# Kernel optimization log

Hardware: AMD Instinct MI355X
Metric: run time of the kernel (lower is better)

Reference implementation:

```python
import jax, jax.numpy as jnp
import numpy as np

N_NODES = 50000
N_EDGES = 800000
D = 256


def setup_inputs() -> dict:
    key = jax.random.key(0)
    k_x, k_e, k_w1, k_w2 = jax.random.split(key, 4)
    x = jax.random.normal(k_x, (N_NODES, D), dtype=jnp.float32)
    edge_index = jax.random.randint(k_e, (2, N_EDGES), 0, N_NODES, dtype=jnp.int64)
    # attention MLP params (Linear(d, d//2) -> ReLU -> Linear(d//2, 1) -> Sigmoid)
    W1 = jax.random.normal(k_w1, (D, D // 2), dtype=jnp.float32) * (1.0 / np.sqrt(D))
    b1 = jnp.zeros((D // 2,), dtype=jnp.float32)
    W2 = jax.random.normal(k_w2, (D // 2, 1), dtype=jnp.float32) * (1.0 / np.sqrt(D // 2))
    b2 = jnp.zeros((1,), dtype=jnp.float32)
    return {"x": x, "edge_index": edge_index, "W1": W1, "b1": b1, "W2": W2, "b2": b2}


def reference(x, edge_index, W1, b1, W2, b2):
    # mean aggregation with attention: for each destination node i (row),
    # weighted mean of neighbor (col) features with sigmoid-MLP attention weights.
    row, col = edge_index[0], edge_index[1]
    neigh = x[col]                                   # [E, D] gathered neighbor features
    h = jax.nn.relu(neigh @ W1 + b1)                 # [E, D//2]
    w = jax.nn.sigmoid(h @ W2 + b2)                  # [E, 1] attention weight per edge
    num = jax.ops.segment_sum(neigh * w, row, num_segments=N_NODES)  # [N, D]
    den = jax.ops.segment_sum(w, row, num_segments=N_NODES)          # [N, 1]
    # nodes with no neighbors stay zero (matching the torch loop's skip)
    out = jnp.where(den > 0, num / jnp.maximum(den, 1e-12), 0.0)
    return out
```

## Files before the change

### kernel.cpp

```cpp
#include <hip/hip_runtime.h>
#include <hip/hip_bf16.h>

#define D 256
#define DH 128
#define NB 8

typedef __attribute__((ext_vector_type(8))) short short8;
typedef __attribute__((ext_vector_type(4))) float floatx4;

__device__ __forceinline__ int eload(const void* p, long long i, int is64) {
    if (is64) return (int)((const long long*)p)[i];
    return ((const int*)p)[i];
}

__device__ __forceinline__ unsigned pack_bf16(unsigned a, unsigned b) {
    unsigned ra = (a + 0x7fffu + ((a >> 16) & 1u)) >> 16;
    unsigned rb = (b + 0x7fffu + ((b >> 16) & 1u)) & 0xffff0000u;
    return ra | rb;
}
__device__ __forceinline__ unsigned short bf16_of(float f) {
    unsigned u = __float_as_uint(f);
    return (unsigned short)((u + 0x7fffu + ((u >> 16) & 1u)) >> 16);
}

__global__ __launch_bounds__(256) void prep_kernel(const float* __restrict__ W1,
                                                   uint4* __restrict__ Bp,
                                                   const int* __restrict__ ei,
                                                   int* __restrict__ flag, int E) {
    if (blockIdx.x == 16) {
        int tid = threadIdx.x;
        int limit = min(E, 4096);
        int v = 0;
        for (int i = tid; i < limit; i += 256) v |= ei[2 * i + 1];
#pragma unroll
        for (int off = 32; off > 0; off >>= 1) v |= __shfl_down(v, off, 64);
        if ((tid & 63) == 0) atomicOr(flag, v);
        return;
    }
    int t = blockIdx.x * 256 + threadIdx.x;
    int lane = t & 63;
    int kt = (t >> 6) & 7;
    int nt = t >> 9;
    int col = nt * 16 + (lane & 15);
    int k0 = kt * 32 + (lane >> 4) * 8;
    unsigned v[8];
#pragma unroll
    for (int j = 0; j < 8; ++j) v[j] = __float_as_uint(W1[(k0 + j) * DH + col]);
    uint4 o;
    o.x = pack_bf16(v[0], v[1]);
    o.y = pack_bf16(v[2], v[3]);
    o.z = pack_bf16(v[4], v[5]);
    o.w = pack_bf16(v[6], v[7]);
    Bp[t] = o;
}

__global__ __launch_bounds__(256) void score_scatter_kernel(
        const float* __restrict__ x, const uint4* __restrict__ Bp,
        const float* __restrict__ b1, const float* __restrict__ W2,
        const float* __restrict__ b2, uint2* __restrict__ xb,
        float* __restrict__ s,
        const void* __restrict__ ep, const int* __restrict__ flag,
        int* __restrict__ cursor, unsigned short* __restrict__ cols,
        int cap, int pad, int N, int E, int SB) {
    if ((int)blockIdx.x >= SB) {
        int is64 = (*flag == 0);
        int base = (blockIdx.x - SB) * 1024 + threadIdx.x;
        int r[4], c[4];
        bool vld[4];
#pragma unroll
        for (int j = 0; j < 4; ++j) {
            int e = base + j * 256;
            vld[j] = (e < E);
            if (vld[j]) {
                r[j] = eload(ep, e, is64);
                c[j] = eload(ep, (long long)E + e, is64);
            }
        }
#pragma unroll
        for (int j = 0; j < 4; ++j) {
            if (vld[j]) {
                int p = atomicAdd(&cursor[r[j] * pad], 1);
                if (p < cap) cols[(size_t)r[j] * cap + p] = (unsigned short)c[j];
            }
        }
        return;
    }

    __shared__ __align__(16) uint2 lds[64 * 65];
    int tid = threadIdx.x;
    int blk = blockIdx.x;
    long long n64 = (long long)N * 64;

    long long gbase = (long long)blk * 4096 + tid;
#pragma unroll
    for (int i = 0; i < 16; ++i) {
        long long g = gbase + i * 256;
        int idx = i * 256 + tid;
        if (g < n64) {
            uint4 f = ((const uint4*)x)[g];
            uint2 o;
            o.x = pack_bf16(f.x, f.y);
            o.y = pack_bf16(f.z, f.w);
            xb[g] = o;
            lds[(idx >> 6) * 65 + (idx & 63)] = o;
        }
    }
    __syncthreads();

    int lane = tid & 63;
    int wid = tid >> 6;
    int quad = lane >> 4;
    int rbase = blk * 64 + wid * 16;
    int lrow = wid * 16 + (lane & 15);

    short8 afrag[8];
#pragma unroll
    for (int kt = 0; kt < 8; ++kt)
        afrag[kt] = *(const short8*)&lds[lrow * 65 + kt * 8 + quad * 2];

    float z0 = 0.f, z1 = 0.f, z2 = 0.f, z3 = 0.f;
#pragma unroll
    for (int nt = 0; nt < 8; ++nt) {
        floatx4 acc = {0.f, 0.f, 0.f, 0.f};
#pragma unroll
        for (int kt = 0; kt < 8; ++kt) {
            uint4 braw = Bp[(nt * 8 + kt) * 64 + lane];
            short8 b;
            b.s0 = (short)(braw.x & 0xffff); b.s1 = (short)(braw.x >> 16);
            b.s2 = (short)(braw.y & 0xffff); b.s3 = (short)(braw.y >> 16);
            b.s4 = (short)(braw.z & 0xffff); b.s5 = (short)(braw.z >> 16);
            b.s6 = (short)(braw.w & 0xffff); b.s7 = (short)(braw.w >> 16);
            acc = __builtin_amdgcn_mfma_f32_16x16x32_bf16(afrag[kt], b, acc, 0, 0, 0);
        }
        int col = nt * 16 + (lane & 15);
        float b1c = b1[col], w2c = W2[col];
        z0 += fmaxf(acc[0] + b1c, 0.f) * w2c;
        z1 += fmaxf(acc[1] + b1c, 0.f) * w2c;
        z2 += fmaxf(acc[2] + b1c, 0.f) * w2c;
        z3 += fmaxf(acc[3] + b1c, 0.f) * w2c;
    }

#pragma unroll
    for (int off = 1; off < 16; off <<= 1) {
        z0 += __shfl_xor(z0, off, 64);
        z1 += __shfl_xor(z1, off, 64);
        z2 += __shfl_xor(z2, off, 64);
        z3 += __shfl_xor(z3, off, 64);
    }
    if ((lane & 15) == 0) {
        float b2v = b2[0];
        int r = rbase + quad * 4;
        float zz[4] = {z0, z1, z2, z3};
#pragma unroll
        for (int j = 0; j < 4; ++j)
            if (r + j < N) s[r + j] = 1.f / (1.f + __expf(-(zz[j] + b2v)));
    }
}

__device__ __forceinline__ float4 unpack_bf16x4(uint2 v) {
    float4 r;
    r.x = __uint_as_float(v.x << 16);
    r.y = __uint_as_float(v.x & 0xffff0000u);
    r.z = __uint_as_float(v.y << 16);
    r.w = __uint_as_float(v.y & 0xffff0000u);
    return r;
}

__global__ __launch_bounds__(256) void agg_u16_kernel(const uint2* __restrict__ xb,
                                                      const float* __restrict__ s,
                                                      const int* __restrict__ cursor,
                                                      const unsigned short* __restrict__ cols,
                                                      int cap, int pad,
                                                      float4* __restrict__ out4, int N) {
    int lane = threadIdx.x & 63;
    int node = blockIdx.x * 4 + (threadIdx.x >> 6);
    if (node >= N) return;
    int cnt = min(cursor[node * pad], cap);
    const unsigned short* mc = cols + (size_t)node * cap;

    float4 acc = make_float4(0.f, 0.f, 0.f, 0.f);
    float den = 0.f;
    int k = 0;
    for (; k + 4 <= cnt; k += 4) {
        int c0 = mc[k], c1 = mc[k + 1], c2 = mc[k + 2], c3 = mc[k + 3];
        float s0 = s[c0], s1 = s[c1], s2 = s[c2], s3 = s[c3];
        uint2 v0 = xb[(size_t)c0 * 64 + lane];
        uint2 v1 = xb[(size_t)c1 * 64 + lane];
        uint2 v2 = xb[(size_t)c2 * 64 + lane];
        uint2 v3 = xb[(size_t)c3 * 64 + lane];
        float4 f0 = unpack_bf16x4(v0);
        float4 f1 = unpack_bf16x4(v1);
        float4 f2 = unpack_bf16x4(v2);
        float4 f3 = unpack_bf16x4(v3);
        acc.x = fmaf(f0.x, s0, fmaf(f1.x, s1, fmaf(f2.x, s2, fmaf(f3.x, s3, acc.x))));
        acc.y = fmaf(f0.y, s0, fmaf(f1.y, s1, fmaf(f2.y, s2, fmaf(f3.y, s3, acc.y))));
        acc.z = fmaf(f0.z, s0, fmaf(f1.z, s1, fmaf(f2.z, s2, fmaf(f3.z, s3, acc.z))));
        acc.w = fmaf(f0.w, s0, fmaf(f1.w, s1, fmaf(f2.w, s2, fmaf(f3.w, s3, acc.w))));
        den += (s0 + s1) + (s2 + s3);
    }
    for (; k < cnt; ++k) {
        int c0 = mc[k];
        float s0 = s[c0];
        float4 f0 = unpack_bf16x4(xb[(size_t)c0 * 64 + lane]);
        acc.x = fmaf(f0.x, s0, acc.x);
        acc.y = fmaf(f0.y, s0, acc.y);
        acc.z = fmaf(f0.z, s0, acc.z);
        acc.w = fmaf(f0.w, s0, acc.w);
        den += s0;
    }
    float4 o = make_float4(0.f, 0.f, 0.f, 0.f);
    if (cnt > 0) {
        float inv = 1.f / den;
        o.x = acc.x * inv; o.y = acc.y * inv; o.z = acc.z * inv; o.w = acc.w * inv;
    }
    out4[(size_t)node * 64 + lane] = o;
}

__global__ __launch_bounds__(256) void detect_kernel(const int* __restrict__ ei,
                                                     int* __restrict__ flag, int E) {
    int tid = threadIdx.x;
    int limit = min(E, 4096);
    int v = 0;
    for (int i = tid; i < limit; i += 256) v |= ei[2 * i + 1];
#pragma unroll
    for (int off = 32; off > 0; off >>= 1) v |= __shfl_down(v, off, 64);
    if ((tid & 63) == 0) atomicOr(flag, v);
}

__global__ __launch_bounds__(256) void score_kernel(const float* __restrict__ x,
                                                    const float* __restrict__ W1,
                                                    const float* __restrict__ b1,
                                                    const float* __restrict__ W2,
                                                    const float* __restrict__ b2,
                                                    float* __restrict__ s, int N) {
    __shared__ __align__(16) float xs[4][NB][D];
    int lane = threadIdx.x & 63;
    int wid  = threadIdx.x >> 6;
    int base = (blockIdx.x * 4 + wid) * NB;
#pragma unroll
    for (int m = 0; m < NB; ++m) {
        int n = base + m;
        float4 v = make_float4(0.f, 0.f, 0.f, 0.f);
        if (n < N) v = ((const float4*)x)[(size_t)n * 64 + lane];
        ((float4*)&xs[wid][m][0])[lane] = v;
    }
    __syncthreads();
    float h0[NB], h1[NB];
#pragma unroll
    for (int m = 0; m < NB; ++m) { h0[m] = 0.f; h1[m] = 0.f; }
#pragma unroll 4
    for (int k = 0; k < D; ++k) {
        float w1a = W1[k * DH + lane];
        float w1b = W1[k * DH + 64 + lane];
#pragma unroll
        for (int m = 0; m < NB; ++m) {
            float xv = xs[wid][m][k];
            h0[m] = fmaf(xv, w1a, h0[m]);
            h1[m] = fmaf(xv, w1b, h1[m]);
        }
    }
    float b1a = b1[lane], b1b = b1[lane + 64];
    float w2a = W2[lane], w2b = W2[lane + 64];
    float b2v = b2[0];
#pragma unroll
    for (int m = 0; m < NB; ++m) {
        float za = fmaxf(h0[m] + b1a, 0.f) * w2a + fmaxf(h1[m] + b1b, 0.f) * w2b;
#pragma unroll
        for (int off = 32; off > 0; off >>= 1) za += __shfl_down(za, off, 64);
        if (lane == 0) {
            int n = base + m;
            if (n < N) s[n] = 1.f / (1.f + __expf(-(za + b2v)));
        }
    }
}

__global__ __launch_bounds__(256) void hist_kernel(const void* __restrict__ ep,
                                                   const int* __restrict__ flag,
                                                   int* __restrict__ cnt, int E) {
    int is64 = (*flag == 0);
    int e = blockIdx.x * blockDim.x + threadIdx.x;
    if (e < E) atomicAdd(&cnt[eload(ep, e, is64)], 1);
}

__global__ __launch_bounds__(256) void bucket_kernel(const int* __restrict__ cnt,
                                                     int* __restrict__ beg,
                                                     int* __restrict__ cursor,
                                                     int* __restrict__ total, int N) {
    int i = blockIdx.x * blockDim.x + threadIdx.x;
    int lane = threadIdx.x & 63;
    int v = (i < N) ? cnt[i] : 0;
    int inc = v;
#pragma unroll
    for (int off = 1; off < 64; off <<= 1) {
        int t = __shfl_up(inc, off, 64);
        if (lane >= off) inc += t;
    }
    int base = 0;
    if (lane == 63) base = atomicAdd(total, inc);
    base = __shfl(base, 63, 64);
    if (i < N) {
        int b = base + inc - v;
        beg[i] = b;
        cursor[i] = b;
    }
}

__global__ __launch_bounds__(256) void scatter32_kernel(const void* __restrict__ ep,
                                                        const int* __restrict__ flag,
                                                        int* __restrict__ cursor,
                                                        int* __restrict__ cols, int E) {
    int is64 = (*flag == 0);
    int e = blockIdx.x * blockDim.x + threadIdx.x;
    if (e < E) {
        int r = eload(ep, e, is64);
        int c = eload(ep, (long long)E + e, is64);
        int p = atomicAdd(&cursor[r], 1);
        cols[p] = c;
    }
}

__global__ __launch_bounds__(256) void agg_f32_kernel(const float4* __restrict__ x4,
                                                      const float* __restrict__ s,
                                                      const int* __restrict__ begs,
                                                      const int* __restrict__ cnt,
                                                      const int* __restrict__ cols,
                                                      float4* __restrict__ out4, int N) {
    int lane = threadIdx.x & 63;
    int node = blockIdx.x * 4 + (threadIdx.x >> 6);
    if (node >= N) return;
    int beg = begs[node], end = beg + cnt[node];
    float4 acc = make_float4(0.f, 0.f, 0.f, 0.f);
    float den = 0.f;
    for (int k = beg; k < end; ++k) {
        int c = cols[k];
        float sc = s[c];
        float4 xv = x4[(size_t)c * 64 + lane];
        acc.x = fmaf(xv.x, sc, acc.x);
        acc.y = fmaf(xv.y, sc, acc.y);
        acc.z = fmaf(xv.z, sc, acc.z);
        acc.w = fmaf(xv.w, sc, acc.w);
        den += sc;
    }
    float4 o = make_float4(0.f, 0.f, 0.f, 0.f);
    if (end > beg) {
        float inv = 1.f / den;
        o.x = acc.x * inv; o.y = acc.y * inv; o.z = acc.z * inv; o.w = acc.w * inv;
    }
    out4[(size_t)node * 64 + lane] = o;
}

extern "C" void kernel_launch(void* const* d_in, const int* in_sizes, int n_in,
                              void* d_out, int out_size, void* d_ws, size_t ws_size,
                              hipStream_t stream) {
    const float* x  = (const float*)d_in[0];
    const void*  ei = d_in[1];
    const float* W1 = (const float*)d_in[2];
    const float* b1 = (const float*)d_in[3];
    const float* W2 = (const float*)d_in[4];
    const float* b2 = (const float*)d_in[5];
    int N = in_sizes[0] / D;
    int E = in_sizes[1] / 2;

    char* ws = (char*)d_ws;

    auto plan = [&](int cap, int pad, size_t& oCur, size_t& oS, size_t& oCols,
                    size_t& oBp, size_t& oXb) -> size_t {
        oCur  = 16;
        oS    = (oCur + (size_t)N * pad * 4 + 15) & ~15ull;
        oCols = (oS + (size_t)N * 4 + 255) & ~255ull;
        oBp   = (oCols + (size_t)N * cap * 2 + 255) & ~255ull;
        oXb   = (oBp + 65536 + 255) & ~255ull;
        return oXb + (size_t)N * D * 2;
    };

    int cap = 96, pad = 16;
    size_t oCur, oS, oCols, oBp, oXb;
    size_t need = plan(cap, pad, oCur, oS, oCols, oBp, oXb);
    if (need > ws_size) { pad = 4;  need = plan(cap, pad, oCur, oS, oCols, oBp, oXb); }
    if (need > ws_size) { pad = 1;  need = plan(cap, pad, oCur, oS, oCols, oBp, oXb); }
    if (need > ws_size) { cap = 64; need = plan(cap, pad, oCur, oS, oCols, oBp, oXb); }

    if (N <= 65536 && need <= ws_size) {
        int*            flag   = (int*)(ws);
        int*            cursor = (int*)(ws + oCur);
        float*          s      = (float*)(ws + oS);
        unsigned short* cols   = (unsigned short*)(ws + oCols);
        uint4*          Bpack  = (uint4*)(ws + oBp);
        uint2*          xb     = (uint2*)(ws + oXb);

        hipMemsetAsync(ws, 0, oCur + (size_t)N * pad * 4, stream);

        prep_kernel<<<17, 256, 0, stream>>>(W1, Bpack, (const int*)ei, flag, E);

        int SB = (N + 63) / 64;
        int TBe = (E + 1023) / 1024;
        score_scatter_kernel<<<SB + TBe, 256, 0, stream>>>(x, Bpack, b1, W2, b2,
                                                           xb, s, ei, flag, cursor,
                                                           cols, cap, pad, N, E, SB);
        agg_u16_kernel<<<(N + 3) / 4, 256, 0, stream>>>(xb, s, cursor, cols, cap, pad,
                                                        (float4*)d_out, N);
        return;
    }

    size_t o0 = 0;
    size_t o1 = 16;
    size_t o2 = (o1 + (size_t)N * 4 + 15) & ~15ull;
    size_t o3 = (o2 + (size_t)N * 4 + 15) & ~15ull;
    size_t o4 = (o3 + (size_t)N * 4 + 15) & ~15ull;
    size_t o5 = (o4 + (size_t)N * 4 + 15) & ~15ull;
    int*   flag   = (int*)(ws + o0);
    int*   total  = (int*)(ws + o0 + 4);
    int*   cnt    = (int*)(ws + o1);
    int*   beg    = (int*)(ws + o2);
    int*   cursor = (int*)(ws + o3);
    float* s      = (float*)(ws + o4);
    int*   cols   = (int*)(ws + o5);

    hipMemsetAsync(ws, 0, o1 + (size_t)N * 4, stream);
    detect_kernel<<<1, 256, 0, stream>>>((const int*)ei, flag, E);
    score_kernel<<<(N + 4 * NB - 1) / (4 * NB), 256, 0, stream>>>(x, W1, b1, W2, b2, s, N);
    hist_kernel<<<(E + 255) / 256, 256, 0, stream>>>(ei, flag, cnt, E);
    bucket_kernel<<<(N + 255) / 256, 256, 0, stream>>>(cnt, beg, cursor, total, N);
    scatter32_kernel<<<(E + 255) / 256, 256, 0, stream>>>(ei, flag, cursor, cols, E);
    agg_f32_kernel<<<(N + 3) / 4, 256, 0, stream>>>((const float4*)x, s, beg, cnt, cols,
                                                    (float4*)d_out, N);
}
```

Measured before the change: 215.3 us.

## Fold cursor zeroing into prep kernel, widen scatter and aggregation unrolls, swizzle LDS

The separate memset is replaced by extra zeroing blocks inside prep_kernel, and the flag is cleared in-kernel. The edge scatter now handles 8 edges per thread with nontemporal column stores. The LDS tile drops its padding column in favour of an XOR swizzle, and B fragments are loaded directly as short8. The aggregation loop adds an 8-wide unroll with vectorized column-index loads and nontemporal output stores. Together these aim to cut a launch, raise memory-level parallelism and reduce instruction overhead, at the cost of more register pressure.

```diff
diff --git a/kernel.cpp b/kernel.cpp
--- a/kernel.cpp
+++ b/kernel.cpp
@@ -7,6 +7,7 @@
 
 typedef __attribute__((ext_vector_type(8))) short short8;
 typedef __attribute__((ext_vector_type(4))) float floatx4;
+typedef __attribute__((ext_vector_type(4))) unsigned int uintx4;
 
 __device__ __forceinline__ int eload(const void* p, long long i, int is64) {
     if (is64) return (int)((const long long*)p)[i];
@@ -26,9 +27,25 @@
 __global__ __launch_bounds__(256) void prep_kernel(const float* __restrict__ W1,
                                                    uint4* __restrict__ Bp,
                                                    const int* __restrict__ ei,
-                                                   int* __restrict__ flag, int E) {
+                                                   int* __restrict__ flag, int E,
+                                                   int* __restrict__ cursor,
+                                                   int N, int pad) {
+    if (blockIdx.x >= 17) {
+        int total4 = (N * pad) >> 2;
+        uint4* c4 = (uint4*)cursor;
+        uint4 z = make_uint4(0u, 0u, 0u, 0u);
+        for (int i = (blockIdx.x - 17) * 256 + threadIdx.x; i < total4;
+             i += (gridDim.x - 17) * 256)
+            c4[i] = z;
+        if (blockIdx.x == 17 && threadIdx.x == 0) {
+            for (int i = total4 * 4; i < N * pad; ++i) cursor[i] = 0;
+        }
+        return;
+    }
     if (blockIdx.x == 16) {
         int tid = threadIdx.x;
+        if (tid == 0) *flag = 0;
+        __syncthreads();
         int limit = min(E, 4096);
         int v = 0;
         for (int i = tid; i < limit; i += 256) v |= ei[2 * i + 1];
@@ -64,11 +81,11 @@
         int cap, int pad, int N, int E, int SB) {
     if ((int)blockIdx.x >= SB) {
         int is64 = (*flag == 0);
-        int base = (blockIdx.x - SB) * 1024 + threadIdx.x;
-        int r[4], c[4];
-        bool vld[4];
-#pragma unroll
-        for (int j = 0; j < 4; ++j) {
+        int base = (blockIdx.x - SB) * 2048 + threadIdx.x;
+        int r[8], c[8];
+        bool vld[8];
+#pragma unroll
+        for (int j = 0; j < 8; ++j) {
             int e = base + j * 256;
             vld[j] = (e < E);
             if (vld[j]) {
@@ -77,16 +94,18 @@
             }
         }
 #pragma unroll
-        for (int j = 0; j < 4; ++j) {
+        for (int j = 0; j < 8; ++j) {
             if (vld[j]) {
                 int p = atomicAdd(&cursor[r[j] * pad], 1);
-                if (p < cap) cols[(size_t)r[j] * cap + p] = (unsigned short)c[j];
+                if (p < cap)
+                    __builtin_nontemporal_store((unsigned short)c[j],
+                                                &cols[(size_t)r[j] * cap + p]);
             }
         }
         return;
     }
 
-    __shared__ __align__(16) uint2 lds[64 * 65];
+    __shared__ __align__(16) uint2 lds[64 * 64];
     int tid = threadIdx.x;
     int blk = blockIdx.x;
     long long n64 = (long long)N * 64;
@@ -102,7 +121,8 @@
             o.x = pack_bf16(f.x, f.y);
             o.y = pack_bf16(f.z, f.w);
             xb[g] = o;
-            lds[(idx >> 6) * 65 + (idx & 63)] = o;
+            int row = idx >> 6, cc = idx & 63;
+            lds[row * 64 + (cc ^ ((row & 7) << 1))] = o;
         }
     }
     __syncthreads();
@@ -112,24 +132,23 @@
     int quad = lane >> 4;
     int rbase = blk * 64 + wid * 16;
     int lrow = wid * 16 + (lane & 15);
+    int fx = (lrow & 7) << 1;
 
     short8 afrag[8];
 #pragma unroll
-    for (int kt = 0; kt < 8; ++kt)
-        afrag[kt] = *(const short8*)&lds[lrow * 65 + kt * 8 + quad * 2];
-
+    for (int kt = 0; kt < 8; ++kt) {
+        int e = kt * 8 + quad * 2;
+        afrag[kt] = *(const short8*)&lds[lrow * 64 + (e ^ fx)];
+    }
+
+    const short8* Bs = (const short8*)Bp;
     float z0 = 0.f, z1 = 0.f, z2 = 0.f, z3 = 0.f;
 #pragma unroll
     for (int nt = 0; nt < 8; ++nt) {
         floatx4 acc = {0.f, 0.f, 0.f, 0.f};
 #pragma unroll
         for (int kt = 0; kt < 8; ++kt) {
-            uint4 braw = Bp[(nt * 8 + kt) * 64 + lane];
-            short8 b;
-            b.s0 = (short)(braw.x & 0xffff); b.s1 = (short)(braw.x >> 16);
-            b.s2 = (short)(braw.y & 0xffff); b.s3 = (short)(braw.y >> 16);
-            b.s4 = (short)(braw.z & 0xffff); b.s5 = (short)(braw.z >> 16);
-            b.s6 = (short)(braw.w & 0xffff); b.s7 = (short)(braw.w >> 16);
+            short8 b = Bs[(nt * 8 + kt) * 64 + lane];
             acc = __builtin_amdgcn_mfma_f32_16x16x32_bf16(afrag[kt], b, acc, 0, 0, 0);
         }
         int col = nt * 16 + (lane & 15);
@@ -181,8 +200,44 @@
     float4 acc = make_float4(0.f, 0.f, 0.f, 0.f);
     float den = 0.f;
     int k = 0;
+    for (; k + 8 <= cnt; k += 8) {
+        uintx4 cc = __builtin_nontemporal_load((const uintx4*)(mc + k));
+        int c0 = cc.x & 0xffff, c1 = cc.x >> 16;
+        int c2 = cc.y & 0xffff, c3 = cc.y >> 16;
+        int c4 = cc.z & 0xffff, c5 = cc.z >> 16;
+        int c6 = cc.w & 0xffff, c7 = cc.w >> 16;
+        float s0 = s[c0], s1 = s[c1], s2 = s[c2], s3 = s[c3];
+        float s4 = s[c4], s5 = s[c5], s6 = s[c6], s7 = s[c7];
+        uint2 v0 = xb[(size_t)c0 * 64 + lane];
+        uint2 v1 = xb[(size_t)c1 * 64 + lane];
+        uint2 v2 = xb[(size_t)c2 * 64 + lane];
+        uint2 v3 = xb[(size_t)c3 * 64 + lane];
+        uint2 v4 = xb[(size_t)c4 * 64 + lane];
+        uint2 v5 = xb[(size_t)c5 * 64 + lane];
+        uint2 v6 = xb[(size_t)c6 * 64 + lane];
+        uint2 v7 = xb[(size_t)c7 * 64 + lane];
+        float4 f0 = unpack_bf16x4(v0);
+        float4 f1 = unpack_bf16x4(v1);
+        float4 f2 = unpack_bf16x4(v2);
+        float4 f3 = unpack_bf16x4(v3);
+        float4 f4 = unpack_bf16x4(v4);
+        float4 f5 = unpack_bf16x4(v5);
+        float4 f6 = unpack_bf16x4(v6);
+        float4 f7 = unpack_bf16x4(v7);
+        acc.x = fmaf(f0.x, s0, fmaf(f1.x, s1, fmaf(f2.x, s2, fmaf(f3.x, s3, acc.x))));
+        acc.y = fmaf(f0.y, s0, fmaf(f1.y, s1, fmaf(f2.y, s2, fmaf(f3.y, s3, acc.y))));
+        acc.z = fmaf(f0.z, s0, fmaf(f1.z, s1, fmaf(f2.z, s2, fmaf(f3.z, s3, acc.z))));
+        acc.w = fmaf(f0.w, s0, fmaf(f1.w, s1, fmaf(f2.w, s2, fmaf(f3.w, s3, acc.w))));
+        acc.x = fmaf(f4.x, s4, fmaf(f5.x, s5, fmaf(f6.x, s6, fmaf(f7.x, s7, acc.x))));
+        acc.y = fmaf(f4.y, s4, fmaf(f5.y, s5, fmaf(f6.y, s6, fmaf(f7.y, s7, acc.y))));
+        acc.z = fmaf(f4.z, s4, fmaf(f5.z, s5, fmaf(f6.z, s6, fmaf(f7.z, s7, acc.z))));
+        acc.w = fmaf(f4.w, s4, fmaf(f5.w, s5, fmaf(f6.w, s6, fmaf(f7.w, s7, acc.w))));
+        den += ((s0 + s1) + (s2 + s3)) + ((s4 + s5) + (s6 + s7));
+    }
     for (; k + 4 <= cnt; k += 4) {
-        int c0 = mc[k], c1 = mc[k + 1], c2 = mc[k + 2], c3 = mc[k + 3];
+        uint2 cc = *(const uint2*)(mc + k);
+        int c0 = cc.x & 0xffff, c1 = cc.x >> 16;
+        int c2 = cc.y & 0xffff, c3 = cc.y >> 16;
         float s0 = s[c0], s1 = s[c1], s2 = s[c2], s3 = s[c3];
         uint2 v0 = xb[(size_t)c0 * 64 + lane];
         uint2 v1 = xb[(size_t)c1 * 64 + lane];
@@ -208,12 +263,12 @@
         acc.w = fmaf(f0.w, s0, acc.w);
         den += s0;
     }
-    float4 o = make_float4(0.f, 0.f, 0.f, 0.f);
+    floatx4 o = {0.f, 0.f, 0.f, 0.f};
     if (cnt > 0) {
         float inv = 1.f / den;
         o.x = acc.x * inv; o.y = acc.y * inv; o.z = acc.z * inv; o.w = acc.w * inv;
     }
-    out4[(size_t)node * 64 + lane] = o;
+    __builtin_nontemporal_store(o, (floatx4*)&out4[(size_t)node * 64 + lane]);
 }
 
 __global__ __launch_bounds__(256) void detect_kernel(const int* __restrict__ ei,
@@ -388,12 +443,12 @@
         uint4*          Bpack  = (uint4*)(ws + oBp);
         uint2*          xb     = (uint2*)(ws + oXb);
 
-        hipMemsetAsync(ws, 0, oCur + (size_t)N * pad * 4, stream);
-
-        prep_kernel<<<17, 256, 0, stream>>>(W1, Bpack, (const int*)ei, flag, E);
+        const int ZB = 256;
+        prep_kernel<<<17 + ZB, 256, 0, stream>>>(W1, Bpack, (const int*)ei, flag, E,
+                                                 cursor, N, pad);
 
         int SB = (N + 63) / 64;
-        int TBe = (E + 1023) / 1024;
+        int TBe = (E + 2047) / 2048;
         score_scatter_kernel<<<SB + TBe, 256, 0, stream>>>(x, Bpack, b1, W2, b2,
                                                            xb, s, ei, flag, cursor,
                                                            cols, cap, pad, N, E, SB);
```

Measured after the change: 205.6 us. 4.5% less time.
